# Kernel optimization log

Hardware: AMD Instinct MI355X
Metric: run time of the kernel (lower is better)

## Reference

```python
import jax, jax.numpy as jnp
import numpy as np

LN_EPS = 1e-5
NUM_HEAD = 8


def _layernorm(x, gamma, beta):
    mu = jnp.mean(x, axis=-1, keepdims=True)
    var = jnp.var(x, axis=-1, keepdims=True)
    return (x - mu) * jax.lax.rsqrt(var + LN_EPS) * gamma + beta


def setup_inputs() -> dict:
    key = jax.random.key(0)
    ks = jax.random.split(key, 5)
    b, T, N, C = 16, 256, 24, 512
    scale = 1.0 / np.sqrt(C)
    return {
        "x": jax.random.normal(ks[0], (b, T, N, C), dtype=jnp.float32),
        "cross_x": jax.random.normal(ks[1], (b, T, N, C), dtype=jnp.float32),
        "gamma": jnp.ones((C,), dtype=jnp.float32),
        "beta": jnp.zeros((C,), dtype=jnp.float32),
        "Wq": (jax.random.normal(ks[2], (C, C), dtype=jnp.float32) * scale),
        "Wk": (jax.random.normal(ks[3], (C, C), dtype=jnp.float32) * scale),
        "Wv": (jax.random.normal(ks[4], (C, C), dtype=jnp.float32) * scale),
    }


def reference(x, cross_x, gamma, beta, Wq, Wk, Wv):
    b, T, N, C = x.shape
    H = NUM_HEAD
    d = C // H
    # fold joints into batch: (b, T, N, C) -> (b*N, T, C)
    xr = jnp.transpose(x, (0, 2, 1, 3)).reshape(b * N, T, C)
    cr = jnp.transpose(cross_x, (0, 2, 1, 3)).reshape(b * N, T, C)
    B = b * N
    xn = _layernorm(xr, gamma, beta)
    cn = _layernorm(cr, gamma, beta)
    # nn.Linear: y = x @ W.T (weight stored [out, in])
    q = jnp.einsum('btc,oc->bto', xn, Wq).reshape(B, T, H, d)
    k = jnp.einsum('btc,oc->bto', cn, Wk).reshape(B, T, H, d)
    v = jnp.einsum('btc,oc->bto', cn, Wv).reshape(B, T, H, d)
    att = jnp.einsum('bnhd,bmhd->bnmh', q, k) / np.sqrt(d).astype(np.float32)
    w = jax.nn.softmax(att, axis=2)  # softmax over key axis m (dropout=0)
    y = jnp.einsum('bnmh,bmhd->bnhd', w, v).reshape(B, T, C)
    y = xr + y
    return jnp.transpose(y.reshape(b, N, T, C), (0, 2, 1, 3))
```

## Files before the change

### kernel.cpp

```cpp
#include <hip/hip_runtime.h>

typedef __bf16 bf16x8 __attribute__((ext_vector_type(8)));
typedef float f32x4 __attribute__((ext_vector_type(4)));

#define MFMA16(a, b, c) __builtin_amdgcn_mfma_f32_16x16x32_bf16(a, b, c, 0, 0, 0)

__device__ __forceinline__ void gload_lds16(const void* g, void* l) {
  __builtin_amdgcn_global_load_lds(
      (const __attribute__((address_space(1))) void*)(unsigned long long)g,
      (__attribute__((address_space(3))) void*)(unsigned int)(unsigned long long)l,
      16, 0, 0);
}

__global__ void cvt_w_kernel(const float* __restrict__ wq, const float* __restrict__ wk,
                             const float* __restrict__ wv, __bf16* __restrict__ w) {
  int i = blockIdx.x * 256 + threadIdx.x;
  w[i]          = (__bf16)wq[i];
  w[i + 262144] = (__bf16)wk[i];
  w[i + 524288] = (__bf16)wv[i];
}

__global__ __launch_bounds__(256) void ln_kernel(
    const float* __restrict__ x, const float* __restrict__ cx,
    const float* __restrict__ g, const float* __restrict__ bet,
    __bf16* __restrict__ xn) {
  int wave = threadIdx.x >> 6, lane = threadIdx.x & 63;
  long row = (long)blockIdx.x * 4 + wave;
  int rloc = (row < 98304) ? (int)row : (int)(row - 98304);
  const float* src = (row < 98304) ? (x + row * 512) : (cx + (long)rloc * 512);
  const f32x4* p = (const f32x4*)(src + lane * 8);
  f32x4 a = p[0], b = p[1];
  float s  = a[0] + a[1] + a[2] + a[3] + b[0] + b[1] + b[2] + b[3];
  float s2 = a[0]*a[0] + a[1]*a[1] + a[2]*a[2] + a[3]*a[3]
           + b[0]*b[0] + b[1]*b[1] + b[2]*b[2] + b[3]*b[3];
  for (int d = 1; d < 64; d <<= 1) { s += __shfl_xor(s, d, 64); s2 += __shfl_xor(s2, d, 64); }
  float mean = s * (1.0f / 512.0f);
  float var  = s2 * (1.0f / 512.0f) - mean * mean;
  float rs = rsqrtf(var + 1e-5f);
  const f32x4* gp = (const f32x4*)(g + lane * 8);
  const f32x4* bp = (const f32x4*)(bet + lane * 8);
  f32x4 g0 = gp[0], g1 = gp[1], b0 = bp[0], b1 = bp[1];
  bf16x8 o;
  for (int j = 0; j < 4; ++j) o[j]     = (__bf16)((a[j] - mean) * rs * g0[j] + b0[j]);
  for (int j = 0; j < 4; ++j) o[4 + j] = (__bf16)((b[j] - mean) * rs * g1[j] + b1[j]);
  int b_ = rloc / 6144;
  int rem = rloc - b_ * 6144;
  int t_ = rem / 24;
  int n_ = rem - t_ * 24;
  long drow = (long)(b_ * 24 + n_) * 256 + t_ + ((row < 98304) ? 0 : 98304);
  *(bf16x8*)(xn + drow * 512 + lane * 8) = o;
}

__global__ __launch_bounds__(256) void gemm_qkv_kernel(
    const __bf16* __restrict__ act, const __bf16* __restrict__ w,
    __bf16* __restrict__ outqkv) {
  int z = blockIdx.z;
  const __bf16* A = act + (z ? (long)50331648 : 0);
  const __bf16* B = w + (long)z * 262144;
  __bf16* C = outqkv + (long)z * 50331648;
  int m0 = blockIdx.x * 128, n0 = blockIdx.y * 128;
  int tid = threadIdx.x, wave = tid >> 6, lane = tid & 63;
  int q4 = lane >> 4, cl = lane & 15;
  int wm = wave & 1, wn = wave >> 1;
  __shared__ __bf16 As[128 * 64];
  __shared__ __bf16 Bs[128 * 64];
  f32x4 acc[4][4] = {};
  for (int kb = 0; kb < 512; kb += 64) {
    for (int i = 0; i < 4; ++i) {
      int t = i * 256 + tid;
      int row = t >> 3;
      int col = (t & 7) * 8;
      gload_lds16(A + (long)(m0 + row) * 512 + kb + col, (char*)As + (i * 256 + wave * 64) * 16);
      gload_lds16(B + (long)(n0 + row) * 512 + kb + col, (char*)Bs + (i * 256 + wave * 64) * 16);
    }
    __syncthreads();
    for (int kc = 0; kc < 2; ++kc) {
      bf16x8 af[4], bfr[4];
      for (int mt = 0; mt < 4; ++mt)
        af[mt] = *(const bf16x8*)(As + (wm * 64 + mt * 16 + cl) * 64 + kc * 32 + q4 * 8);
      for (int nt = 0; nt < 4; ++nt)
        bfr[nt] = *(const bf16x8*)(Bs + (wn * 64 + nt * 16 + cl) * 64 + kc * 32 + q4 * 8);
      for (int mt = 0; mt < 4; ++mt)
        for (int nt = 0; nt < 4; ++nt)
          acc[mt][nt] = MFMA16(af[mt], bfr[nt], acc[mt][nt]);
    }
    __syncthreads();
  }
  for (int mt = 0; mt < 4; ++mt)
    for (int nt = 0; nt < 4; ++nt) {
      int col = n0 + wn * 64 + nt * 16 + cl;
      int hh = col >> 6, dd = col & 63;
      int mbase = m0 + wm * 64 + mt * 16 + q4 * 4;
      for (int r = 0; r < 4; ++r) {
        int m = mbase + r;
        long addr = ((long)((m >> 8) * 8 + hh) << 14) + ((m & 255) << 6) + dd;
        C[addr] = (__bf16)acc[mt][nt][r];
      }
    }
}

__global__ __launch_bounds__(256) void attn_kernel(
    const __bf16* __restrict__ Q, const __bf16* __restrict__ K,
    const __bf16* __restrict__ V, const float* __restrict__ x,
    float* __restrict__ out) {
  int blk = blockIdx.x;
  int h = blk & 7;
  int bn = blk >> 3;
  int n_ = bn % 24;
  int b_ = bn / 24;
  const __bf16* Qh = Q + (long)blk * 16384;
  const __bf16* Kh = K + (long)blk * 16384;
  const __bf16* Vh = V + (long)blk * 16384;
  long xbase = (long)b_ * 3145728 + (long)n_ * 512 + h * 64;

  int tid = threadIdx.x, wave = tid >> 6, lane = tid & 63;
  int q4 = lane >> 4, cl = lane & 15;

  __shared__ __bf16 Ks[256 * 64];
  __shared__ __bf16 Vt[64 * 256];

  {
    int c = lane & 7;
    int r8 = lane >> 3;
    for (int it = 0; it < 8; ++it) {
      int row = wave * 64 + it * 8 + r8;
      gload_lds16(Kh + row * 64 + ((c ^ (row & 7)) << 3),
                  (char*)Ks + (wave * 64 + it * 8) * 128);
    }
  }
  {
    int key = tid;
    int colp = (key & ~31) | ((key & 12) << 1) | ((key & 16) >> 2) | (key & 3);
    const __bf16* vrow = Vh + key * 64;
    for (int i = 0; i < 8; ++i) {
      bf16x8 v = *(const bf16x8*)(vrow + i * 8);
      for (int j = 0; j < 8; ++j) {
        int d = i * 8 + j;
        *(__bf16*)((char*)Vt + d * 512 + ((colp * 2) ^ ((d & 7) << 4))) = v[j];
      }
    }
  }
  __syncthreads();

  const float c_exp = 0.125f * 1.44269504088896f;
  for (int iter = 0; iter < 4; ++iter) {
    int qt = wave * 4 + iter;
    const __bf16* qrow = Qh + (qt * 16 + cl) * 64 + q4 * 8;
    bf16x8 qb0 = *(const bf16x8*)(qrow);
    bf16x8 qb1 = *(const bf16x8*)(qrow + 32);
    f32x4 s[16];
#pragma unroll
    for (int kt = 0; kt < 16; ++kt) {
      int row = kt * 16 + cl;
      const char* kb = (const char*)Ks + row * 128;
      bf16x8 ka0 = *(const bf16x8*)(kb + ((q4 ^ (row & 7)) << 4));
      bf16x8 ka1 = *(const bf16x8*)(kb + (((4 + q4) ^ (row & 7)) << 4));
      f32x4 a = {};
      a = MFMA16(ka0, qb0, a);
      a = MFMA16(ka1, qb1, a);
      s[kt] = a;
    }
    float mx = -1e30f;
#pragma unroll
    for (int kt = 0; kt < 16; ++kt)
#pragma unroll
      for (int r = 0; r < 4; ++r) mx = fmaxf(mx, s[kt][r]);
    mx = fmaxf(mx, __shfl_xor(mx, 16, 64));
    mx = fmaxf(mx, __shfl_xor(mx, 32, 64));
    float lsum = 0.0f;
#pragma unroll
    for (int kt = 0; kt < 16; ++kt)
#pragma unroll
      for (int r = 0; r < 4; ++r) {
        float p = exp2f((s[kt][r] - mx) * c_exp);
        s[kt][r] = p;
        lsum += p;
      }
    lsum += __shfl_xor(lsum, 16, 64);
    lsum += __shfl_xor(lsum, 32, 64);

    f32x4 o[4] = {};
#pragma unroll
    for (int m = 0; m < 8; ++m) {
      bf16x8 pa;
#pragma unroll
      for (int j = 0; j < 4; ++j) {
        pa[j]     = (__bf16)s[2 * m][j];
        pa[4 + j] = (__bf16)s[2 * m + 1][j];
      }
#pragma unroll
      for (int db = 0; db < 4; ++db) {
        int row = db * 16 + cl;
        bf16x8 vb = *(const bf16x8*)((const char*)Vt + row * 512 +
                                     (((m * 4 + q4) ^ (row & 7)) << 4));
        o[db] = MFMA16(pa, vb, o[db]);
      }
    }
#pragma unroll
    for (int r = 0; r < 4; ++r) {
      float lr = __shfl(lsum, q4 * 4 + r, 64);
      float inv = 1.0f / lr;
      long trow = xbase + (long)(qt * 16 + q4 * 4 + r) * 12288;
#pragma unroll
      for (int db = 0; db < 4; ++db) {
        long addr = trow + db * 16 + cl;
        out[addr] = x[addr] + o[db][r] * inv;
      }
    }
  }
}

extern "C" void kernel_launch(void* const* d_in, const int* in_sizes, int n_in,
                              void* d_out, int out_size, void* d_ws, size_t ws_size,
                              hipStream_t stream) {
  const float* x     = (const float*)d_in[0];
  const float* cx    = (const float*)d_in[1];
  const float* gamma = (const float*)d_in[2];
  const float* beta  = (const float*)d_in[3];
  const float* Wq    = (const float*)d_in[4];
  const float* Wk    = (const float*)d_in[5];
  const float* Wv    = (const float*)d_in[6];
  float* out = (float*)d_out;
  char* ws = (char*)d_ws;

  __bf16* Wb = (__bf16*)(ws);
  __bf16* xn = (__bf16*)(ws + 1572864);
  __bf16* Qb = (__bf16*)(ws + 202899456);

  cvt_w_kernel<<<1024, 256, 0, stream>>>(Wq, Wk, Wv, Wb);
  ln_kernel<<<49152, 256, 0, stream>>>(x, cx, gamma, beta, xn);
  gemm_qkv_kernel<<<dim3(768, 4, 3), 256, 0, stream>>>(xn, Wb, Qb);
  attn_kernel<<<3072, 256, 0, stream>>>(Qb, Qb + 50331648, Qb + 100663296, x, out);
}
```

Measured before the change: 1.161 ms.

## Stream K from global with online softmax, pad V transpose in LDS

Rewrites the attention kernel to drop the K staging in LDS and read K fragments straight from global/L2. The score tile is now processed in four key chunks with an online (flash-style) softmax that rescales the accumulator when the running max grows. The XOR-swizzled V-transpose layout is replaced by a padded row layout, and launch bounds request 4 blocks per CU. The intent is to cut registers and LDS per block to raise occupancy; the cost is repeated uncached-in-LDS K loads and extra rescale work.

```diff
diff --git a/kernel.cpp b/kernel.cpp
--- a/kernel.cpp
+++ b/kernel.cpp
@@ -99,7 +99,7 @@
     }
 }
 
-__global__ __launch_bounds__(256) void attn_kernel(
+__global__ __launch_bounds__(256, 4) void attn_kernel(
     const __bf16* __restrict__ Q, const __bf16* __restrict__ K,
     const __bf16* __restrict__ V, const float* __restrict__ x,
     float* __restrict__ out) {
@@ -116,28 +116,15 @@
   int tid = threadIdx.x, wave = tid >> 6, lane = tid & 63;
   int q4 = lane >> 4, cl = lane & 15;
 
-  __shared__ __bf16 Ks[256 * 64];
-  __shared__ __bf16 Vt[64 * 256];
-
-  {
-    int c = lane & 7;
-    int r8 = lane >> 3;
-    for (int it = 0; it < 8; ++it) {
-      int row = wave * 64 + it * 8 + r8;
-      gload_lds16(Kh + row * 64 + ((c ^ (row & 7)) << 3),
-                  (char*)Ks + (wave * 64 + it * 8) * 128);
-    }
-  }
+  __shared__ __align__(16) __bf16 Vt[64][264];
+
   {
     int key = tid;
     int colp = (key & ~31) | ((key & 12) << 1) | ((key & 16) >> 2) | (key & 3);
     const __bf16* vrow = Vh + key * 64;
     for (int i = 0; i < 8; ++i) {
       bf16x8 v = *(const bf16x8*)(vrow + i * 8);
-      for (int j = 0; j < 8; ++j) {
-        int d = i * 8 + j;
-        *(__bf16*)((char*)Vt + d * 512 + ((colp * 2) ^ ((d & 7) << 4))) = v[j];
-      }
+      for (int j = 0; j < 8; ++j) Vt[i * 8 + j][colp] = v[j];
     }
   }
   __syncthreads();
@@ -148,57 +135,66 @@
     const __bf16* qrow = Qh + (qt * 16 + cl) * 64 + q4 * 8;
     bf16x8 qb0 = *(const bf16x8*)(qrow);
     bf16x8 qb1 = *(const bf16x8*)(qrow + 32);
-    f32x4 s[16];
-#pragma unroll
-    for (int kt = 0; kt < 16; ++kt) {
-      int row = kt * 16 + cl;
-      const char* kb = (const char*)Ks + row * 128;
-      bf16x8 ka0 = *(const bf16x8*)(kb + ((q4 ^ (row & 7)) << 4));
-      bf16x8 ka1 = *(const bf16x8*)(kb + (((4 + q4) ^ (row & 7)) << 4));
-      f32x4 a = {};
-      a = MFMA16(ka0, qb0, a);
-      a = MFMA16(ka1, qb1, a);
-      s[kt] = a;
-    }
-    float mx = -1e30f;
-#pragma unroll
-    for (int kt = 0; kt < 16; ++kt)
-#pragma unroll
-      for (int r = 0; r < 4; ++r) mx = fmaxf(mx, s[kt][r]);
-    mx = fmaxf(mx, __shfl_xor(mx, 16, 64));
-    mx = fmaxf(mx, __shfl_xor(mx, 32, 64));
-    float lsum = 0.0f;
-#pragma unroll
-    for (int kt = 0; kt < 16; ++kt)
+    f32x4 o[4] = {};
+    float m = -1e30f, l = 0.0f;
+#pragma unroll
+    for (int c = 0; c < 4; ++c) {
+      f32x4 s4[4];
+#pragma unroll
+      for (int kk = 0; kk < 4; ++kk) {
+        const __bf16* krow = Kh + ((c * 4 + kk) * 16 + cl) * 64 + q4 * 8;
+        bf16x8 ka0 = *(const bf16x8*)(krow);
+        bf16x8 ka1 = *(const bf16x8*)(krow + 32);
+        f32x4 a = {};
+        a = MFMA16(ka0, qb0, a);
+        a = MFMA16(ka1, qb1, a);
+        s4[kk] = a;
+      }
+      float cm = -1e30f;
+#pragma unroll
+      for (int kk = 0; kk < 4; ++kk)
+#pragma unroll
+        for (int r = 0; r < 4; ++r) cm = fmaxf(cm, s4[kk][r]);
+      cm = fmaxf(cm, __shfl_xor(cm, 16, 64));
+      cm = fmaxf(cm, __shfl_xor(cm, 32, 64));
+      if (!__all(cm <= m)) {
+        float mn = fmaxf(m, cm);
+        float sc = exp2f((m - mn) * c_exp);
+        m = mn;
+        l *= sc;
+        float s0 = __shfl(sc, q4 * 4 + 0, 64);
+        float s1 = __shfl(sc, q4 * 4 + 1, 64);
+        float s2 = __shfl(sc, q4 * 4 + 2, 64);
+        float s3 = __shfl(sc, q4 * 4 + 3, 64);
+#pragma unroll
+        for (int db = 0; db < 4; ++db) {
+          o[db][0] *= s0; o[db][1] *= s1; o[db][2] *= s2; o[db][3] *= s3;
+        }
+      }
+      bf16x8 pa0, pa1;
 #pragma unroll
       for (int r = 0; r < 4; ++r) {
-        float p = exp2f((s[kt][r] - mx) * c_exp);
-        s[kt][r] = p;
-        lsum += p;
-      }
-    lsum += __shfl_xor(lsum, 16, 64);
-    lsum += __shfl_xor(lsum, 32, 64);
-
-    f32x4 o[4] = {};
-#pragma unroll
-    for (int m = 0; m < 8; ++m) {
-      bf16x8 pa;
-#pragma unroll
-      for (int j = 0; j < 4; ++j) {
-        pa[j]     = (__bf16)s[2 * m][j];
-        pa[4 + j] = (__bf16)s[2 * m + 1][j];
+        float p0 = exp2f((s4[0][r] - m) * c_exp);
+        float p1 = exp2f((s4[1][r] - m) * c_exp);
+        float p2 = exp2f((s4[2][r] - m) * c_exp);
+        float p3 = exp2f((s4[3][r] - m) * c_exp);
+        l += (p0 + p1) + (p2 + p3);
+        pa0[r] = (__bf16)p0; pa0[4 + r] = (__bf16)p1;
+        pa1[r] = (__bf16)p2; pa1[4 + r] = (__bf16)p3;
       }
 #pragma unroll
       for (int db = 0; db < 4; ++db) {
-        int row = db * 16 + cl;
-        bf16x8 vb = *(const bf16x8*)((const char*)Vt + row * 512 +
-                                     (((m * 4 + q4) ^ (row & 7)) << 4));
-        o[db] = MFMA16(pa, vb, o[db]);
-      }
-    }
+        bf16x8 vb0 = *(const bf16x8*)(&Vt[db * 16 + cl][c * 64 + q4 * 8]);
+        bf16x8 vb1 = *(const bf16x8*)(&Vt[db * 16 + cl][c * 64 + 32 + q4 * 8]);
+        o[db] = MFMA16(pa0, vb0, o[db]);
+        o[db] = MFMA16(pa1, vb1, o[db]);
+      }
+    }
+    l += __shfl_xor(l, 16, 64);
+    l += __shfl_xor(l, 32, 64);
 #pragma unroll
     for (int r = 0; r < 4; ++r) {
-      float lr = __shfl(lsum, q4 * 4 + r, 64);
+      float lr = __shfl(l, q4 * 4 + r, 64);
       float inv = 1.0f / lr;
       long trow = xbase + (long)(qt * 16 + q4 * 4 + r) * 12288;
 #pragma unroll
```

Result: slower. 1.484 ms (+27.8%).
